# Performance work log

Hardware: AMD Instinct MI355X
Metric: run time of the kernel (lower is better)

Reference implementation:

```python
import jax, jax.numpy as jnp
import numpy as np

N, E, D_IN, H, C, N_GRAPHS = 50000, 800000, 128, 2, 64, 50
D_HID = H * C  # 128
NEG_SLOPE = 0.2
EPS = 1e-16


def glorot(key, shape):
    fan_in, fan_out = shape[0], shape[-1]
    lim = jnp.sqrt(6.0 / (fan_in + fan_out))
    return jax.random.uniform(key, shape, jnp.float32, -lim, lim)


def setup_inputs() -> dict:
    key = jax.random.key(0)
    ks = jax.random.split(key, 12)
    x = jax.random.normal(ks[0], (N, D_IN), jnp.float32)
    edge_index = jax.random.randint(ks[1], (2, E), 0, N, jnp.int64)
    batch = jnp.sort(jax.random.randint(ks[2], (N,), 0, N_GRAPHS, jnp.int64))
    # GATConv layer 1: in=128 -> heads=2, out=64
    W1 = glorot(ks[3], (D_IN, H * C))
    as1 = glorot(ks[4], (1, H, C)).reshape(H, C)
    ad1 = glorot(ks[5], (1, H, C)).reshape(H, C)
    b1 = jnp.zeros((H * C,), jnp.float32)
    # GATConv layer 2: in=128 -> heads=2, out=64
    W2 = glorot(ks[6], (D_HID, H * C))
    as2 = glorot(ks[7], (1, H, C)).reshape(H, C)
    ad2 = glorot(ks[8], (1, H, C)).reshape(H, C)
    b2 = jnp.zeros((H * C,), jnp.float32)
    # Linear head: 128 -> 1
    Wh = glorot(ks[9], (D_HID, 1))
    bh = jnp.zeros((1,), jnp.float32)
    return {"x": x, "edge_index": edge_index, "batch": batch,
            "W1": W1, "as1": as1, "ad1": ad1, "b1": b1,
            "W2": W2, "as2": as2, "ad2": ad2, "b2": b2,
            "Wh": Wh, "bh": bh}


def gat_conv(x, src, dst, W, a_src, a_dst, bias):
    # PyG GATConv (concat=True, add_self_loops applied by caller, eval mode)
    n = x.shape[0]
    h = (x @ W).reshape(n, H, C)                       # [N,H,C]
    al_s = jnp.einsum('nhc,hc->nh', h, a_src)          # [N,H]
    al_d = jnp.einsum('nhc,hc->nh', h, a_dst)
    e = jax.nn.leaky_relu(al_s[src] + al_d[dst], NEG_SLOPE)  # [E',H]
    # segment softmax over incoming edges of each dst node
    e_max = jax.ops.segment_max(e, dst, num_segments=n)
    e = jnp.exp(e - e_max[dst])
    denom = jax.ops.segment_sum(e, dst, num_segments=n)
    alpha = e / (denom[dst] + EPS)                     # [E',H]
    out = jax.ops.segment_sum(alpha[:, :, None] * h[src], dst, num_segments=n)
    return out.reshape(n, H * C) + bias


def reference(x, edge_index, batch, W1, as1, ad1, b1, W2, as2, ad2, b2, Wh, bh):
    # add self-loops (PyG GATConv default)
    loops = jnp.arange(N, dtype=edge_index.dtype)
    src = jnp.concatenate([edge_index[0], loops])
    dst = jnp.concatenate([edge_index[1], loops])
    h = gat_conv(x, src, dst, W1, as1, ad1, b1)
    h = jax.nn.relu(h)  # dropout is identity in eval mode
    h = gat_conv(h, src, dst, W2, as2, ad2, b2)
    h = jax.nn.relu(h)
    # global mean pool over graphs
    sums = jax.ops.segment_sum(h, batch, num_segments=N_GRAPHS)
    counts = jax.ops.segment_sum(jnp.ones((N, 1), h.dtype), batch, num_segments=N_GRAPHS)
    pooled = sums / jnp.maximum(counts, 1.0)           # [G, 128]
    return pooled @ Wh + bh                            # [G, 1]
```

## Files before the change

### kernel.cpp

```cpp
#include <hip/hip_runtime.h>
#include <hip/hip_fp16.h>
#include <math.h>

#define HD 128
#define NEG_SLOPE 0.2f
#define EPSV 1e-16f
#define TILE 8192

typedef unsigned short ushort_t;
typedef __attribute__((ext_vector_type(8))) short bf16x8;
typedef __attribute__((ext_vector_type(8))) _Float16 f16x8;
typedef __attribute__((ext_vector_type(4))) float f32x4;

__device__ inline void bsplit(float x, ushort_t& hi, ushort_t& lo) {
    unsigned u = __float_as_uint(x);
    hi = (ushort_t)(u >> 16);
    float res = x - __uint_as_float(u & 0xffff0000u);
    unsigned v = __float_as_uint(res);
    lo = (ushort_t)((v + 0x7FFFu + ((v >> 16) & 1u)) >> 16);
}

__global__ __launch_bounds__(256) void pre_build(const int* __restrict__ dst,
                                                 int* __restrict__ tileHist, int E, int NT,
                                                 const float* __restrict__ W1,
                                                 const float* __restrict__ W2,
                                                 ushort_t* __restrict__ Whs1,
                                                 ushort_t* __restrict__ Wls1,
                                                 ushort_t* __restrict__ Whs2,
                                                 ushort_t* __restrict__ Wls2) {
    int t = threadIdx.x;
    if ((int)blockIdx.x < NT) {
        __shared__ int hist[256];
        hist[t] = 0;
        __syncthreads();
        int base = blockIdx.x * TILE;
        int end = base + TILE; if (end > E) end = E;
        for (int i = base + t; i < end; i += 256)
            atomicAdd(&hist[dst[i] >> 8], 1);
        __syncthreads();
        tileHist[blockIdx.x * 256 + t] = hist[t];
        return;
    }
    int blk = blockIdx.x - NT;
    bool layer2 = blk >= 64;
    int idx = (blk & 63) * 256 + t;
    int j    = idx & 7;
    int lane = (idx >> 3) & 63;
    int ks   = (idx >> 9) & 3;
    int ct   = idx >> 11;
    int n = ct * 16 + (lane & 15);
    int k = ks * 32 + (lane >> 4) * 8 + j;
    if (!layer2) {
        ushort_t hi, lo;
        bsplit(W1[k * 128 + n], hi, lo);
        Whs1[idx] = hi;
        Wls1[idx] = lo;
    } else {
        float v = W2[k * 128 + n];
        __half h = __float2half(v);
        __half l = __float2half(v - __half2float(h));
        Whs2[idx] = __half_as_ushort(h);
        Wls2[idx] = __half_as_ushort(l);
    }
}

__global__ __launch_bounds__(256) void part_offsets(int* __restrict__ tileHist,
                                                    int* __restrict__ bucketBase,
                                                    int NT) {
    __shared__ int s[256];
    int b = threadIdx.x;
    int total = 0;
    #pragma unroll 8
    for (int t = 0; t < NT; ++t) total += tileHist[t * 256 + b];
    s[b] = total;
    __syncthreads();
    for (int o = 1; o < 256; o <<= 1) {
        int v = (b >= o) ? s[b - o] : 0;
        __syncthreads();
        s[b] += v;
        __syncthreads();
    }
    int base = (b == 0) ? 0 : s[b - 1];
    bucketBase[b] = base;
    if (b == 255) bucketBase[256] = s[255];
    int run = base;
    #pragma unroll 8
    for (int t = 0; t < NT; ++t) {
        int v = tileHist[t * 256 + b];
        tileHist[t * 256 + b] = run;
        run += v;
    }
}

__global__ __launch_bounds__(256) void part_scatter(const int* __restrict__ src,
                                                    const int* __restrict__ dst,
                                                    const int* __restrict__ tileHist,
                                                    int* __restrict__ part, int E) {
    __shared__ int cur[256];
    int t = threadIdx.x;
    cur[t] = tileHist[blockIdx.x * 256 + t];
    __syncthreads();
    int base = blockIdx.x * TILE;
    int end = base + TILE; if (end > E) end = E;
    for (int i = base + t; i < end; i += 256) {
        int d = dst[i], s = src[i];
        int p = atomicAdd(&cur[d >> 8], 1);
        part[p] = (s << 8) | (d & 255);
    }
}

__global__ __launch_bounds__(256) void csr_build(const int* __restrict__ part,
                                                 const int* __restrict__ bucketBase,
                                                 int* __restrict__ indptr,
                                                 int* __restrict__ csr, int N, int E) {
    __shared__ int hist[256];
    __shared__ int pfx[256];
    __shared__ int cur[256];
    int t = threadIdx.x;
    int b = blockIdx.x;
    hist[t] = 0;
    __syncthreads();
    int s0 = bucketBase[b], s1 = bucketBase[b + 1];
    for (int i = s0 + t; i < s1; i += 256)
        atomicAdd(&hist[part[i] & 255], 1);
    __syncthreads();
    pfx[t] = hist[t];
    __syncthreads();
    for (int o = 1; o < 256; o <<= 1) {
        int u = (t >= o) ? pfx[t - o] : 0;
        __syncthreads();
        pfx[t] += u;
        __syncthreads();
    }
    int excl = (t == 0) ? 0 : pfx[t - 1];
    int d = b * 256 + t;
    int ip = s0 + excl + d;
    if (d < N) indptr[d] = ip;
    if (b == 0 && t == 0) indptr[N] = E + N;
    cur[t] = ip;
    __syncthreads();
    for (int i = s0 + t; i < s1; i += 256) {
        int e = part[i];
        int p = atomicAdd(&cur[e & 255], 1);
        csr[p] = e >> 8;
    }
    __syncthreads();
    if (d < N) csr[cur[t]] = d;
}

__global__ __launch_bounds__(256) void gemm_mfma(const float* __restrict__ A,
                                                 const ushort_t* __restrict__ Whs,
                                                 const ushort_t* __restrict__ Wls,
                                                 const float* __restrict__ a_s,
                                                 const float* __restrict__ a_d,
                                                 __half* __restrict__ h16,
                                                 float* __restrict__ als,
                                                 float* __restrict__ ald, int N) {
    const int gw   = (blockIdx.x * 256 + threadIdx.x) >> 6;
    const int lane = threadIdx.x & 63;
    const int r0   = gw * 16;
    if (r0 >= N) return;
    const int m = lane & 15;
    const int q = lane >> 4;

    bf16x8 ah[4], al[4];
    {
        int row = r0 + m;
        if (row >= N) row = N - 1;
        const float* ap = A + (size_t)row * HD;
        #pragma unroll
        for (int ks = 0; ks < 4; ++ks) {
            float4 v0 = *(const float4*)(ap + ks * 32 + q * 8);
            float4 v1 = *(const float4*)(ap + ks * 32 + q * 8 + 4);
            float vv[8] = {v0.x, v0.y, v0.z, v0.w, v1.x, v1.y, v1.z, v1.w};
            #pragma unroll
            for (int j = 0; j < 8; ++j) {
                ushort_t hb, lb;
                bsplit(vv[j], hb, lb);
                ah[ks][j] = (short)hb;
                al[ks][j] = (short)lb;
            }
        }
    }

    float ps[4] = {0,0,0,0};
    float pd[4] = {0,0,0,0};

    #pragma unroll 1
    for (int ct = 0; ct < 8; ++ct) {
        f32x4 acc = {0.f, 0.f, 0.f, 0.f};
        #pragma unroll
        for (int ks = 0; ks < 4; ++ks) {
            bf16x8 wh = *(const bf16x8*)(Whs + ((size_t)(ct * 4 + ks) * 64 + lane) * 8);
            bf16x8 wl = *(const bf16x8*)(Wls + ((size_t)(ct * 4 + ks) * 64 + lane) * 8);
            acc = __builtin_amdgcn_mfma_f32_16x16x32_bf16(ah[ks], wh, acc, 0, 0, 0);
            acc = __builtin_amdgcn_mfma_f32_16x16x32_bf16(al[ks], wh, acc, 0, 0, 0);
            acc = __builtin_amdgcn_mfma_f32_16x16x32_bf16(ah[ks], wl, acc, 0, 0, 0);
        }
        const int col = ct * 16 + m;
        const float asv = a_s[col], adv = a_d[col];
        #pragma unroll
        for (int reg = 0; reg < 4; ++reg) {
            ps[reg] += acc[reg] * asv;
            pd[reg] += acc[reg] * adv;
            int row = r0 + q * 4 + reg;
            if (row < N) h16[(size_t)row * HD + col] = __float2half(acc[reg]);
        }
        if (ct == 3 || ct == 7) {
            int head = ct >> 2;
            #pragma unroll
            for (int reg = 0; reg < 4; ++reg) {
                float vs = ps[reg], vd = pd[reg];
                for (int o = 8; o >= 1; o >>= 1) {
                    vs += __shfl_xor(vs, o, 64);
                    vd += __shfl_xor(vd, o, 64);
                }
                if (m == 0) {
                    int row = r0 + q * 4 + reg;
                    if (row < N) { als[2 * row + head] = vs; ald[2 * row + head] = vd; }
                }
                ps[reg] = 0.f;  pd[reg] = 0.f;
            }
        }
    }
}

__global__ __launch_bounds__(256) void gemm_mfma_f16(const __half* __restrict__ A,
                                                     const ushort_t* __restrict__ Whs,
                                                     const ushort_t* __restrict__ Wls,
                                                     const float* __restrict__ a_s,
                                                     const float* __restrict__ a_d,
                                                     __half* __restrict__ h16,
                                                     float* __restrict__ als,
                                                     float* __restrict__ ald, int N) {
    const int gw   = (blockIdx.x * 256 + threadIdx.x) >> 6;
    const int lane = threadIdx.x & 63;
    const int r0   = gw * 16;
    if (r0 >= N) return;
    const int m = lane & 15;
    const int q = lane >> 4;

    f16x8 ah[4];
    {
        int row = r0 + m;
        if (row >= N) row = N - 1;
        const __half* ap = A + (size_t)row * HD;
        #pragma unroll
        for (int ks = 0; ks < 4; ++ks)
            ah[ks] = *(const f16x8*)(ap + ks * 32 + q * 8);
    }

    float ps[4] = {0,0,0,0};
    float pd[4] = {0,0,0,0};

    #pragma unroll 1
    for (int ct = 0; ct < 8; ++ct) {
        f32x4 acc = {0.f, 0.f, 0.f, 0.f};
        #pragma unroll
        for (int ks = 0; ks < 4; ++ks) {
            f16x8 wh = *(const f16x8*)(Whs + ((size_t)(ct * 4 + ks) * 64 + lane) * 8);
            f16x8 wl = *(const f16x8*)(Wls + ((size_t)(ct * 4 + ks) * 64 + lane) * 8);
            acc = __builtin_amdgcn_mfma_f32_16x16x32_f16(ah[ks], wh, acc, 0, 0, 0);
            acc = __builtin_amdgcn_mfma_f32_16x16x32_f16(ah[ks], wl, acc, 0, 0, 0);
        }
        const int col = ct * 16 + m;
        const float asv = a_s[col], adv = a_d[col];
        #pragma unroll
        for (int reg = 0; reg < 4; ++reg) {
            ps[reg] += acc[reg] * asv;
            pd[reg] += acc[reg] * adv;
            int row = r0 + q * 4 + reg;
            if (row < N) h16[(size_t)row * HD + col] = __float2half(acc[reg]);
        }
        if (ct == 3 || ct == 7) {
            int head = ct >> 2;
            #pragma unroll
            for (int reg = 0; reg < 4; ++reg) {
                float vs = ps[reg], vd = pd[reg];
                for (int o = 8; o >= 1; o >>= 1) {
                    vs += __shfl_xor(vs, o, 64);
                    vd += __shfl_xor(vd, o, 64);
                }
                if (m == 0) {
                    int row = r0 + q * 4 + reg;
                    if (row < N) { als[2 * row + head] = vs; ald[2 * row + head] = vd; }
                }
                ps[reg] = 0.f;  pd[reg] = 0.f;
            }
        }
    }
}

__global__ __launch_bounds__(256) void gat_aggregate(const __half* __restrict__ h,
                                                     const float* __restrict__ als,
                                                     const float* __restrict__ ald,
                                                     const int* __restrict__ indptr,
                                                     const int* __restrict__ csr,
                                                     const float* __restrict__ bias,
                                                     __half* __restrict__ out,
                                                     const float* __restrict__ Wh,
                                                     float* __restrict__ svec, int N) {
    __shared__ int2 ebuf[4][64];
    int w    = (blockIdx.x * blockDim.x + threadIdx.x) >> 6;
    int lane = threadIdx.x & 63;
    int wv   = (threadIdx.x >> 6);
    if (w >= N) return;
    int start = indptr[w], end = indptr[w + 1];
    float ad0 = ald[2 * w], ad1 = ald[2 * w + 1];
    const bool head0 = (lane < 32);
    const int cbase = lane * 2;

    float accx = 0.f, accy = 0.f, dsum = 0.f;
    for (int base = start; base < end; base += 64) {
        int i = base + lane;
        int idx = i < end ? i : end - 1;
        int s = csr[idx];
        unsigned wpack = 0u;
        if (i < end) {
            float2 av = *(const float2*)&als[2 * s];
            float e0 = av.x + ad0;
            float e1 = av.y + ad1;
            e0 = e0 > 0.f ? e0 : NEG_SLOPE * e0;
            e1 = e1 > 0.f ? e1 : NEG_SLOPE * e1;
            __half p0 = __float2half(__expf(e0));
            __half p1 = __float2half(__expf(e1));
            wpack = ((unsigned)__half_as_ushort(p1) << 16) | __half_as_ushort(p0);
        }
        ebuf[wv][lane] = make_int2(s, (int)wpack);
        int nl = end - base; if (nl > 64) nl = 64;
        int nb = (nl + 7) >> 3;
        for (int b = 0; b < nb; ++b) {
            int j = b * 8;
            int2 e[8];
            #pragma unroll
            for (int u = 0; u < 8; ++u) e[u] = ebuf[wv][j + u];
            float wa[8];
            #pragma unroll
            for (int u = 0; u < 8; ++u) {
                unsigned wp = (unsigned)e[u].y;
                unsigned bits = head0 ? (wp & 0xffffu) : (wp >> 16);
                wa[u] = __half2float(__ushort_as_half((ushort_t)bits));
            }
            __half2 hv[8];
            #pragma unroll
            for (int u = 0; u < 8; ++u)
                hv[u] = *(const __half2*)&h[(size_t)e[u].x * HD + cbase];
            #pragma unroll
            for (int u = 0; u < 8; ++u) {
                float2 f = __half22float2(hv[u]);
                dsum += wa[u];
                accx += wa[u] * f.x;
                accy += wa[u] * f.y;
            }
        }
    }
    float D = dsum + EPSV;
    float ox = accx / D + bias[cbase];
    float oy = accy / D + bias[cbase + 1];
    ox = ox > 0.f ? ox : 0.f;
    oy = oy > 0.f ? oy : 0.f;

    if (svec) {
        float2 wv2 = *(const float2*)&Wh[cbase];
        float part = ox * wv2.x + oy * wv2.y;
        for (int o = 32; o >= 1; o >>= 1) part += __shfl_xor(part, o, 64);
        if (lane == 0) svec[w] = part;
    } else {
        *(__half2*)&out[(size_t)w * HD + cbase] =
            __halves2half2(__float2half(ox), __float2half(oy));
    }
}

__global__ __launch_bounds__(256) void pool_head(const float* __restrict__ s,
                                                 const int* __restrict__ batch,
                                                 const float* __restrict__ bh,
                                                 float* __restrict__ out, int N, int G) {
    __shared__ float partial[4];
    int g = blockIdx.x, t = threadIdx.x;
    auto lb = [&](int key) {
        int lo = 0, hi = N;
        while (lo < hi) {
            int mid = (lo + hi) >> 1;
            if (batch[mid] < key) lo = mid + 1; else hi = mid;
        }
        return lo;
    };
    int a = lb(g), b = lb(g + 1);
    float sum = 0.f;
    for (int i = a + t; i < b; i += 256) sum += s[i];
    for (int o = 32; o >= 1; o >>= 1) sum += __shfl_xor(sum, o, 64);
    if ((t & 63) == 0) partial[t >> 6] = sum;
    __syncthreads();
    if (t == 0) {
        float cnt = (float)(b - a); if (cnt < 1.f) cnt = 1.f;
        out[g] = (partial[0] + partial[1] + partial[2] + partial[3]) / cnt + bh[0];
    }
}

extern "C" void kernel_launch(void* const* d_in, const int* in_sizes, int n_in,
                              void* d_out, int out_size, void* d_ws, size_t ws_size,
                              hipStream_t stream) {
    const float* x     = (const float*)d_in[0];
    const int*   ei    = (const int*)d_in[1];
    const int*   batch = (const int*)d_in[2];
    const float* W1  = (const float*)d_in[3];
    const float* as1 = (const float*)d_in[4];
    const float* ad1 = (const float*)d_in[5];
    const float* b1  = (const float*)d_in[6];
    const float* W2  = (const float*)d_in[7];
    const float* as2 = (const float*)d_in[8];
    const float* ad2 = (const float*)d_in[9];
    const float* b2  = (const float*)d_in[10];
    const float* Wh  = (const float*)d_in[11];
    const float* bh  = (const float*)d_in[12];
    float* out = (float*)d_out;

    const int N = in_sizes[0] / HD;
    const int E = in_sizes[1] / 2;
    const int G = out_size;
    const int* srcp = ei;
    const int* dstp = ei + E;
    const int NBK = (N + 255) / 256;
    const int NT  = (E + TILE - 1) / TILE;

    char* ws = (char*)d_ws;
    size_t off = 0;
    auto alloc = [&](size_t bytes) -> void* {
        void* p = ws + off;
        off += (bytes + 255) & ~(size_t)255;
        return p;
    };
    __half* h16   = (__half*)alloc((size_t)N * HD * 2);
    __half* ob16  = (__half*)alloc((size_t)N * HD * 2);
    float* als    = (float*)alloc((size_t)N * 2 * 4);
    float* ald    = (float*)alloc((size_t)N * 2 * 4);
    float* svec   = (float*)alloc((size_t)N * 4);
    int*   indptr = (int*)  alloc((size_t)(N + 1) * 4);
    int*   csr    = (int*)  alloc((size_t)(E + N) * 4);
    int*   tileHist   = (int*)alloc((size_t)NT * 256 * 4);
    int*   bucketBase = (int*)alloc(257 * 4);
    int*   part   = (int*)  alloc((size_t)E * 4);
    ushort_t* Whs1 = (ushort_t*)alloc(16384 * 2);
    ushort_t* Wls1 = (ushort_t*)alloc(16384 * 2);
    ushort_t* Whs2 = (ushort_t*)alloc(16384 * 2);
    ushort_t* Wls2 = (ushort_t*)alloc(16384 * 2);

    pre_build<<<NT + 128, 256, 0, stream>>>(dstp, tileHist, E, NT,
                                            W1, W2, Whs1, Wls1, Whs2, Wls2);
    part_offsets<<<1, 256, 0, stream>>>(tileHist, bucketBase, NT);
    part_scatter<<<NT, 256, 0, stream>>>(srcp, dstp, tileHist, part, E);
    csr_build<<<NBK, 256, 0, stream>>>(part, bucketBase, indptr, csr, N, E);

    const int nwaves  = (N + 15) / 16;
    const int gblocks = (nwaves + 3) / 4;
    int wgrid = (N * 64 + 255) / 256;

    gemm_mfma<<<gblocks, 256, 0, stream>>>(x, Whs1, Wls1, as1, ad1, h16, als, ald, N);
    gat_aggregate<<<wgrid, 256, 0, stream>>>(h16, als, ald, indptr, csr, b1, ob16,
                                             nullptr, nullptr, N);
    gemm_mfma_f16<<<gblocks, 256, 0, stream>>>(ob16, Whs2, Wls2, as2, ad2, h16,
                                               als, ald, N);
    gat_aggregate<<<wgrid, 256, 0, stream>>>(h16, als, ald, indptr, csr, b2, nullptr,
                                             Wh, svec, N);
    pool_head<<<G, 256, 0, stream>>>(svec, batch, bh, out, N, G);
}
```

Measured before the change: 248.6 us.

## Parallelize bucket offset scan and split aggregate wave into two edge groups

```diff
diff --git a/kernel.cpp b/kernel.cpp
--- a/kernel.cpp
+++ b/kernel.cpp
@@ -64,41 +64,48 @@
     }
 }
 
-__global__ __launch_bounds__(256) void part_offsets(int* __restrict__ tileHist,
-                                                    int* __restrict__ bucketBase,
-                                                    int NT) {
+__global__ __launch_bounds__(256) void bucket_scan(int* __restrict__ tileHist,
+                                                   int* __restrict__ bucketTotal, int NT) {
     __shared__ int s[256];
-    int b = threadIdx.x;
-    int total = 0;
-    #pragma unroll 8
-    for (int t = 0; t < NT; ++t) total += tileHist[t * 256 + b];
-    s[b] = total;
+    int t = threadIdx.x, b = blockIdx.x;
+    int v = (t < NT) ? tileHist[t * 256 + b] : 0;
+    s[t] = v;
     __syncthreads();
     for (int o = 1; o < 256; o <<= 1) {
-        int v = (b >= o) ? s[b - o] : 0;
-        __syncthreads();
-        s[b] += v;
-        __syncthreads();
-    }
-    int base = (b == 0) ? 0 : s[b - 1];
-    bucketBase[b] = base;
-    if (b == 255) bucketBase[256] = s[255];
-    int run = base;
-    #pragma unroll 8
-    for (int t = 0; t < NT; ++t) {
-        int v = tileHist[t * 256 + b];
-        tileHist[t * 256 + b] = run;
-        run += v;
-    }
+        int u = (t >= o) ? s[t - o] : 0;
+        __syncthreads();
+        s[t] += u;
+        __syncthreads();
+    }
+    int excl = (t == 0) ? 0 : s[t - 1];
+    if (t < NT) tileHist[t * 256 + b] = excl;
+    if (t == 255) bucketTotal[b] = s[255];
+}
+
+__global__ __launch_bounds__(256) void bucket_base(const int* __restrict__ bucketTotal,
+                                                   int* __restrict__ bucketBase) {
+    __shared__ int s[256];
+    int t = threadIdx.x;
+    s[t] = bucketTotal[t];
+    __syncthreads();
+    for (int o = 1; o < 256; o <<= 1) {
+        int u = (t >= o) ? s[t - o] : 0;
+        __syncthreads();
+        s[t] += u;
+        __syncthreads();
+    }
+    bucketBase[t] = (t == 0) ? 0 : s[t - 1];
+    if (t == 255) bucketBase[256] = s[255];
 }
 
 __global__ __launch_bounds__(256) void part_scatter(const int* __restrict__ src,
                                                     const int* __restrict__ dst,
                                                     const int* __restrict__ tileHist,
+                                                    const int* __restrict__ bucketBase,
                                                     int* __restrict__ part, int E) {
     __shared__ int cur[256];
     int t = threadIdx.x;
-    cur[t] = tileHist[blockIdx.x * 256 + t];
+    cur[t] = tileHist[blockIdx.x * 256 + t] + bucketBase[t];
     __syncthreads();
     int base = blockIdx.x * TILE;
     int end = base + TILE; if (end > E) end = E;
@@ -307,10 +314,12 @@
     if (w >= N) return;
     int start = indptr[w], end = indptr[w + 1];
     float ad0 = ald[2 * w], ad1 = ald[2 * w + 1];
-    const bool head0 = (lane < 32);
-    const int cbase = lane * 2;
-
-    float accx = 0.f, accy = 0.f, dsum = 0.f;
+    const int sl = lane & 31;
+    const int g  = lane >> 5;
+    const int c0 = sl * 4;
+    const bool headlo = (sl < 16);
+
+    float a0 = 0.f, a1 = 0.f, a2 = 0.f, a3 = 0.f, dsum = 0.f;
     for (int base = start; base < end; base += 64) {
         int i = base + lane;
         int idx = i < end ? i : end - 1;
@@ -328,46 +337,60 @@
         }
         ebuf[wv][lane] = make_int2(s, (int)wpack);
         int nl = end - base; if (nl > 64) nl = 64;
-        int nb = (nl + 7) >> 3;
-        for (int b = 0; b < nb; ++b) {
-            int j = b * 8;
+        int nit = (nl + 15) >> 4;
+        for (int b = 0; b < nit; ++b) {
+            int j = b * 16 + g;
             int2 e[8];
             #pragma unroll
-            for (int u = 0; u < 8; ++u) e[u] = ebuf[wv][j + u];
+            for (int u = 0; u < 8; ++u) e[u] = ebuf[wv][j + 2 * u];
             float wa[8];
             #pragma unroll
             for (int u = 0; u < 8; ++u) {
                 unsigned wp = (unsigned)e[u].y;
-                unsigned bits = head0 ? (wp & 0xffffu) : (wp >> 16);
+                unsigned bits = headlo ? (wp & 0xffffu) : (wp >> 16);
                 wa[u] = __half2float(__ushort_as_half((ushort_t)bits));
             }
-            __half2 hv[8];
+            uint2 hv[8];
             #pragma unroll
             for (int u = 0; u < 8; ++u)
-                hv[u] = *(const __half2*)&h[(size_t)e[u].x * HD + cbase];
+                hv[u] = *(const uint2*)&h[(size_t)e[u].x * HD + c0];
             #pragma unroll
             for (int u = 0; u < 8; ++u) {
-                float2 f = __half22float2(hv[u]);
+                float2 f01 = __half22float2(*(__half2*)&hv[u].x);
+                float2 f23 = __half22float2(*(__half2*)&hv[u].y);
                 dsum += wa[u];
-                accx += wa[u] * f.x;
-                accy += wa[u] * f.y;
+                a0 += wa[u] * f01.x;
+                a1 += wa[u] * f01.y;
+                a2 += wa[u] * f23.x;
+                a3 += wa[u] * f23.y;
             }
         }
     }
+    dsum += __shfl_xor(dsum, 32, 64);
+    a0 += __shfl_xor(a0, 32, 64);
+    a1 += __shfl_xor(a1, 32, 64);
+    a2 += __shfl_xor(a2, 32, 64);
+    a3 += __shfl_xor(a3, 32, 64);
     float D = dsum + EPSV;
-    float ox = accx / D + bias[cbase];
-    float oy = accy / D + bias[cbase + 1];
-    ox = ox > 0.f ? ox : 0.f;
-    oy = oy > 0.f ? oy : 0.f;
+    float o0 = a0 / D + bias[c0 + 0];
+    float o1 = a1 / D + bias[c0 + 1];
+    float o2 = a2 / D + bias[c0 + 2];
+    float o3 = a3 / D + bias[c0 + 3];
+    o0 = o0 > 0.f ? o0 : 0.f;
+    o1 = o1 > 0.f ? o1 : 0.f;
+    o2 = o2 > 0.f ? o2 : 0.f;
+    o3 = o3 > 0.f ? o3 : 0.f;
 
     if (svec) {
-        float2 wv2 = *(const float2*)&Wh[cbase];
-        float part = ox * wv2.x + oy * wv2.y;
-        for (int o = 32; o >= 1; o >>= 1) part += __shfl_xor(part, o, 64);
+        const float4 wv4 = *(const float4*)&Wh[c0];
+        float part = o0 * wv4.x + o1 * wv4.y + o2 * wv4.z + o3 * wv4.w;
+        for (int o = 16; o >= 1; o >>= 1) part += __shfl_xor(part, o, 64);
         if (lane == 0) svec[w] = part;
-    } else {
-        *(__half2*)&out[(size_t)w * HD + cbase] =
-            __halves2half2(__float2half(ox), __float2half(oy));
+    } else if (g == 0) {
+        uint2 pack;
+        *(__half2*)&pack.x = __halves2half2(__float2half(o0), __float2half(o1));
+        *(__half2*)&pack.y = __halves2half2(__float2half(o2), __float2half(o3));
+        *(uint2*)&out[(size_t)w * HD + c0] = pack;
     }
 }
 
@@ -437,8 +460,9 @@
     float* svec   = (float*)alloc((size_t)N * 4);
     int*   indptr = (int*)  alloc((size_t)(N + 1) * 4);
     int*   csr    = (int*)  alloc((size_t)(E + N) * 4);
-    int*   tileHist   = (int*)alloc((size_t)NT * 256 * 4);
-    int*   bucketBase = (int*)alloc(257 * 4);
+    int*   tileHist    = (int*)alloc((size_t)NT * 256 * 4);
+    int*   bucketTotal = (int*)alloc(256 * 4);
+    int*   bucketBase  = (int*)alloc(257 * 4);
     int*   part   = (int*)  alloc((size_t)E * 4);
     ushort_t* Whs1 = (ushort_t*)alloc(16384 * 2);
     ushort_t* Wls1 = (ushort_t*)alloc(16384 * 2);
@@ -447,8 +471,9 @@
 
     pre_build<<<NT + 128, 256, 0, stream>>>(dstp, tileHist, E, NT,
                                             W1, W2, Whs1, Wls1, Whs2, Wls2);
-    part_offsets<<<1, 256, 0, stream>>>(tileHist, bucketBase, NT);
-    part_scatter<<<NT, 256, 0, stream>>>(srcp, dstp, tileHist, part, E);
+    bucket_scan<<<256, 256, 0, stream>>>(tileHist, bucketTotal, NT);
+    bucket_base<<<1, 256, 0, stream>>>(bucketTotal, bucketBase);
+    part_scatter<<<NT, 256, 0, stream>>>(srcp, dstp, tileHist, bucketBase, part, E);
     csr_build<<<NBK, 256, 0, stream>>>(part, bucketBase, indptr, csr, N, E);
 
     const int nwaves  = (N + 15) / 16;
```

Measured after the change: 252.9 us. No clear change (+1.7%).
